# Optimization experiments

Measured on AMD Instinct MI355X. Metric: run time of the kernel, lower is better.

## Reference

```python
import jax, jax.numpy as jnp
import numpy as np

B, S, T, H, VS, VE = 32, 128, 128, 512, 8000, 8000


def _lstm_scan(x_proj, W_hh, bias, h0, c0):
    # x_proj: [L, B, 4H] precomputed input projections; gate order i,f,g,o (PyTorch)
    def step(carry, xp):
        h, c = carry
        gates = xp + h @ W_hh.T + bias  # [B, 4H]
        i, f, g, o = jnp.split(gates, 4, axis=-1)
        c = jax.nn.sigmoid(f) * c + jax.nn.sigmoid(i) * jnp.tanh(g)
        h = jax.nn.sigmoid(o) * jnp.tanh(c)
        return (h, c), h
    (h, c), hs = jax.lax.scan(step, (h0, c0), x_proj)
    return hs, h, c


def setup_inputs() -> dict:
    key = jax.random.key(0)
    ks = jax.random.split(key, 16)
    sc_h = 1.0 / np.sqrt(H)
    u = lambda k, shape: jax.random.uniform(k, shape, jnp.float32, -sc_h, sc_h)
    return {
        "input_batch": jax.random.randint(ks[0], (B, S), 0, VS),
        "output_batch": jax.random.randint(ks[1], (B, T), 0, VE),
        "Wa": u(ks[2], (H, H)), "ba": u(ks[3], (H,)),
        "W1": u(ks[4], (H, 2 * H)), "b1": u(ks[5], (H,)),
        "W2": u(ks[6], (VE, H)), "b2": u(ks[7], (VE,)),
        "We_ih": u(ks[8], (4 * H, VS)), "We_hh": u(ks[9], (4 * H, H)),
        "be_ih": u(ks[10], (4 * H,)), "be_hh": u(ks[11], (4 * H,)),
        "Wd_ih": u(ks[12], (4 * H, VE)), "Wd_hh": u(ks[13], (4 * H, H)),
        "bd_ih": u(ks[14], (4 * H,)), "bd_hh": u(ks[15], (4 * H,)),
    }


def reference(input_batch, output_batch, Wa, ba, W1, b1, W2, b2,
              We_ih, We_hh, be_ih, be_hh, Wd_ih, Wd_hh, bd_ih, bd_hh):
    src = input_batch.T  # [S, B]
    tgt = output_batch.T  # [T, B]
    # one_hot(tok) @ W_ih.T  ==  W_ih.T[tok]  (gather instead of dense one-hot GEMM)
    enc_xp = jnp.take(We_ih.T, src, axis=0)  # [S, B, 4H]
    dec_xp = jnp.take(Wd_ih.T, tgt, axis=0)  # [T, B, 4H]
    h0 = jnp.zeros((B, H), jnp.float32)
    c0 = jnp.zeros((B, H), jnp.float32)
    enc_outputs, h, c = _lstm_scan(enc_xp, We_hh, be_ih + be_hh, h0, c0)  # [S,B,H]
    proj_enc = enc_outputs @ Wa.T + ba  # attn(enc_outputs): [S, B, H]
    dec_bias = bd_ih + bd_hh

    def dec_step(carry, xp):
        h, c = carry
        gates = xp + h @ Wd_hh.T + dec_bias
        i, f, g, o = jnp.split(gates, 4, axis=-1)
        c = jax.nn.sigmoid(f) * c + jax.nn.sigmoid(i) * jnp.tanh(g)
        h = jax.nn.sigmoid(o) * jnp.tanh(c)  # [B, H] == dec_output
        scores = jnp.einsum('sbh,bh->bs', proj_enc, h)  # [B, S]
        w = jax.nn.softmax(scores, axis=1)
        context = jnp.einsum('bs,sbh->bh', w, enc_outputs)  # [B, H]
        hid = jnp.tanh(jnp.concatenate([h, context], axis=1) @ W1.T + b1)
        logits = hid @ W2.T + b2  # [B, VE]
        return (h, c), logits

    _, model = jax.lax.scan(dec_step, (h, c), dec_xp)  # [T, B, VE]
    return jax.nn.softmax(model.transpose(1, 0, 2), axis=2)  # [B, T, VE]
```

## Files before the change

### kernel.cpp

```cpp
#include <hip/hip_runtime.h>
#include <hip/hip_cooperative_groups.h>

#define NB 32
#define NS 128
#define NT 128
#define NH 512
#define NVS 8000
#define NVE 8000

typedef float fx4 __attribute__((ext_vector_type(4)));
typedef short bf16x8 __attribute__((ext_vector_type(8)));
typedef float f32x4 __attribute__((ext_vector_type(4)));

__device__ __forceinline__ float sigm(float x) { return 1.0f / (1.0f + expf(-x)); }

__device__ __forceinline__ fx4 load_cg(const float* p) {
  fx4 v;
  asm volatile("global_load_dwordx4 %0, %1, off sc0 sc1" : "=v"(v) : "v"(p));
  return v;
}
__device__ __forceinline__ void store_cg(float* p, fx4 v) {
  asm volatile("global_store_dwordx4 %0, %1, off sc0 sc1" :: "v"(p), "v"(v) : "memory");
}

__global__ __launch_bounds__(256) void scan_kernel(
    const int* __restrict__ in_tok, const int* __restrict__ out_tok,
    const float* __restrict__ We_ih, const float* __restrict__ We_hh,
    const float* __restrict__ be_ih, const float* __restrict__ be_hh,
    const float* __restrict__ Wd_ih, const float* __restrict__ Wd_hh,
    const float* __restrict__ bd_ih, const float* __restrict__ bd_hh,
    float* __restrict__ h_buf,
    float* __restrict__ enc_out,
    float* __restrict__ dec_h,
    int* __restrict__ flags)
{
  __shared__ float W_lds[16][520];
  __shared__ float h_lds[16 * 516];
  __shared__ float gbuf[16][16];
  __shared__ float c_buf[4][16];
  __shared__ float hstage[16][4];

  const int tid = threadIdx.x;
  const int g   = blockIdx.x;
  const int bg  = g & 1;
  const int mg  = g >> 1;
  const int r   = tid >> 4;
  const int bl  = tid & 15;
  const int b   = bg * 16 + bl;
  const int q   = r >> 2;
  const int i   = r & 3;
  const int j   = q * NH + mg * 4 + i;

  const float bias_e = be_ih[j] + be_hh[j];
  const float bias_d = bd_ih[j] + bd_hh[j];
  const float* Wcol_e = We_ih + (size_t)j * NVS;
  const float* Wcol_d = Wd_ih + (size_t)j * NVE;

  if (tid < 64) c_buf[tid >> 4][tid & 15] = 0.0f;

  {
    const float* Wg = We_hh;
    for (int u = tid; u < 2048; u += 256) {
      const int rr = u >> 7;
      const int k4 = (u & 127) << 2;
      const int jj = (rr >> 2) * NH + mg * 4 + (rr & 3);
      *(float4*)&W_lds[rr][k4] = *(const float4*)(Wg + (size_t)jj * NH + k4);
    }
  }
  __syncthreads();

  for (int s = 0; s < NS + NT; ++s) {
    const bool enc = (s < NS);
    if (s == NS) {
      const float* Wg = Wd_hh;
      for (int u = tid; u < 2048; u += 256) {
        const int rr = u >> 7;
        const int k4 = (u & 127) << 2;
        const int jj = (rr >> 2) * NH + mg * 4 + (rr & 3);
        *(float4*)&W_lds[rr][k4] = *(const float4*)(Wg + (size_t)jj * NH + k4);
      }
      __syncthreads();
    }
    const int st  = enc ? s : s - NS;
    const int tok = enc ? in_tok[b * NS + st] : out_tok[b * NT + st];
    const float xp = enc ? Wcol_e[tok] : Wcol_d[tok];
    const float bias = enc ? bias_e : bias_d;
    const float* Wrow = &W_lds[r][0];

    float acc = 0.0f;
    if (s > 0) {
      if (tid < 128) {
        const int idx = (tid << 1) | bg;
        while (__hip_atomic_load(&flags[idx], __ATOMIC_RELAXED,
                                 __HIP_MEMORY_SCOPE_AGENT) < s)
          __builtin_amdgcn_s_sleep(1);
      }
      __syncthreads();
      const float* hsrc = h_buf + ((s - 1) & 1) * (NB * NH) + bg * 16 * NH;
      fx4 tmp[8];
      #pragma unroll
      for (int it = 0; it < 8; ++it)
        tmp[it] = load_cg(hsrc + ((tid + (it << 8)) << 2));
      asm volatile("s_waitcnt vmcnt(0)" ::: "memory");
      __builtin_amdgcn_sched_barrier(0);
      #pragma unroll
      for (int it = 0; it < 8; ++it) {
        const int u = tid + (it << 8);
        const int bb = u >> 7;
        const int kk = (u & 127) << 2;
        *(fx4*)&h_lds[bb * 516 + kk] = tmp[it];
      }
      __syncthreads();
      const float* hrow = &h_lds[bl * 516];
      #pragma unroll 8
      for (int k = 0; k < NH; k += 4) {
        const float4 hv = *(const float4*)(hrow + k);
        const float4 wv = *(const float4*)(Wrow + k);
        acc += hv.x * wv.x + hv.y * wv.y + hv.z * wv.z + hv.w * wv.w;
      }
    }
    gbuf[r][bl] = acc + xp + bias;
    __syncthreads();

    if (tid < 64) {
      const int ii = tid >> 4;
      const int bb = tid & 15;
      const float gi = gbuf[ii][bb];
      const float gf = gbuf[4 + ii][bb];
      const float gg = gbuf[8 + ii][bb];
      const float go = gbuf[12 + ii][bb];
      const float co = c_buf[ii][bb];
      const float cn = sigm(gf) * co + sigm(gi) * tanhf(gg);
      const float hn = sigm(go) * tanhf(cn);
      c_buf[ii][bb] = cn;
      hstage[bb][ii] = hn;
    }
    __syncthreads();
    if (tid < 16) {
      const fx4 hv = *(const fx4*)&hstage[tid][0];
      const int bglob = bg * 16 + tid;
      store_cg(h_buf + (s & 1) * (NB * NH) + bglob * NH + mg * 4, hv);
      float* dst = enc ? (enc_out + ((size_t)st * NB + bglob) * NH + mg * 4)
                       : (dec_h  + ((size_t)st * NB + bglob) * NH + mg * 4);
      *(fx4*)dst = hv;
    }
    asm volatile("s_waitcnt vmcnt(0)" ::: "memory");
    __syncthreads();
    if (tid == 0)
      __hip_atomic_store(&flags[g], s + 1, __ATOMIC_RELAXED,
                         __HIP_MEMORY_SCOPE_AGENT);
  }
}

template<int TRANSB, int CSWAP, int ACT>
__global__ __launch_bounds__(256) void gemm64(
    const float* __restrict__ A, const float* __restrict__ Bm,
    float* __restrict__ C, const float* __restrict__ bias,
    const float* __restrict__ A2, int ksplit,
    int M, int N, int K, int lda, int ldb, int ldc,
    long batchA, long batchB, long batchC)
{
  __shared__ float As[16][68];
  __shared__ float Bs[16][68];
  const int z = blockIdx.z;
  A += (long)z * batchA;
  if (A2 != nullptr) A2 += (long)z * batchA;
  Bm += (long)z * batchB;
  C  += (long)z * batchC;
  const int m0 = blockIdx.y << 6;
  const int n0 = blockIdx.x << 6;
  const int tid = threadIdx.x;
  const int tx = tid & 15;
  const int ty = tid >> 4;
  float acc[4][4] = {};

  for (int k0 = 0; k0 < K; k0 += 16) {
    {
      const int mrow = tid >> 2;
      const int kcq = (tid & 3) << 2;
      const float* base = A;
      int keff = k0;
      if (A2 != nullptr && k0 >= ksplit) { base = A2; keff = k0 - ksplit; }
      const float4 v = *(const float4*)(base + (long)(m0 + mrow) * lda + keff + kcq);
      As[kcq + 0][mrow] = v.x; As[kcq + 1][mrow] = v.y;
      As[kcq + 2][mrow] = v.z; As[kcq + 3][mrow] = v.w;
    }
    if (TRANSB == 0) {
      const int nrow = tid >> 2;
      const int kcq = (tid & 3) << 2;
      const float4 v = *(const float4*)(Bm + (long)(n0 + nrow) * ldb + k0 + kcq);
      Bs[kcq + 0][nrow] = v.x; Bs[kcq + 1][nrow] = v.y;
      Bs[kcq + 2][nrow] = v.z; Bs[kcq + 3][nrow] = v.w;
    } else {
      const int krow = tid >> 4;
      const int nc = (tid & 15) << 2;
      const float4 v = *(const float4*)(Bm + (long)(k0 + krow) * ldb + n0 + nc);
      *(float4*)&Bs[krow][nc] = v;
    }
    __syncthreads();
    #pragma unroll
    for (int kk = 0; kk < 16; ++kk) {
      const float4 a4 = *(const float4*)&As[kk][ty << 2];
      const float4 b4 = *(const float4*)&Bs[kk][tx << 2];
      const float a[4]  = {a4.x, a4.y, a4.z, a4.w};
      const float bv[4] = {b4.x, b4.y, b4.z, b4.w};
      #pragma unroll
      for (int ii = 0; ii < 4; ++ii)
        #pragma unroll
        for (int jj = 0; jj < 4; ++jj)
          acc[ii][jj] = fmaf(a[ii], bv[jj], acc[ii][jj]);
    }
    __syncthreads();
  }

  const int n = n0 + (tx << 2);
  float4 bb4 = {0.f, 0.f, 0.f, 0.f};
  if (bias) { bb4.x = bias[n]; bb4.y = bias[n + 1]; bb4.z = bias[n + 2]; bb4.w = bias[n + 3]; }
  #pragma unroll
  for (int ii = 0; ii < 4; ++ii) {
    const int mrow = m0 + (ty << 2) + ii;
    float4 o;
    o.x = acc[ii][0] + bb4.x; o.y = acc[ii][1] + bb4.y;
    o.z = acc[ii][2] + bb4.z; o.w = acc[ii][3] + bb4.w;
    if (ACT == 1) { o.x = tanhf(o.x); o.y = tanhf(o.y); o.z = tanhf(o.z); o.w = tanhf(o.w); }
    long orow = mrow;
    if (CSWAP) orow = (long)(mrow & (NB - 1)) * NT + (mrow >> 5);
    *(float4*)(C + orow * (long)ldc + n) = o;
  }
}

template<int CSWAP, int ACT>
__global__ __launch_bounds__(256) void gemm128db(
    const float* __restrict__ A, const float* __restrict__ Bm,
    float* __restrict__ C, const float* __restrict__ bias,
    const float* __restrict__ A2, int ksplit,
    int M, int N, int K, int lda, int ldb, int ldc)
{
  __shared__ float As[2][16][132];
  __shared__ float Bs[2][16][68];
  const int m0 = blockIdx.y << 7;
  const int n0 = blockIdx.x << 6;
  const int tid = threadIdx.x;
  const int tx = tid & 15;
  const int ty = tid >> 4;
  const int mrow = tid >> 1;
  const int kq   = (tid & 1) << 3;
  const int nrow = tid >> 2;
  const int kqb  = (tid & 3) << 2;
  float acc[8][4] = {};

  float4 va0, va1, vb;
  {
    const float* base = A;
    int keff = 0;
    if (A2 != nullptr && 0 >= ksplit) { base = A2; keff = -ksplit; }
    const float* p = base + (long)(m0 + mrow) * lda + keff + kq;
    va0 = *(const float4*)(p);
    va1 = *(const float4*)(p + 4);
    vb  = *(const float4*)(Bm + (long)(n0 + nrow) * ldb + kqb);
  }
  {
    As[0][kq + 0][mrow] = va0.x; As[0][kq + 1][mrow] = va0.y;
    As[0][kq + 2][mrow] = va0.z; As[0][kq + 3][mrow] = va0.w;
    As[0][kq + 4][mrow] = va1.x; As[0][kq + 5][mrow] = va1.y;
    As[0][kq + 6][mrow] = va1.z; As[0][kq + 7][mrow] = va1.w;
    Bs[0][kqb + 0][nrow] = vb.x; Bs[0][kqb + 1][nrow] = vb.y;
    Bs[0][kqb + 2][nrow] = vb.z; Bs[0][kqb + 3][nrow] = vb.w;
  }
  __syncthreads();

  const int T = K >> 4;
  for (int t = 0; t < T; ++t) {
    const int cur = t & 1;
    if (t + 1 < T) {
      const int k0 = (t + 1) << 4;
      const float* base = A;
      int keff = k0;
      if (A2 != nullptr && k0 >= ksplit) { base = A2; keff = k0 - ksplit; }
      const float* p = base + (long)(m0 + mrow) * lda + keff + kq;
      va0 = *(const float4*)(p);
      va1 = *(const float4*)(p + 4);
      vb  = *(const float4*)(Bm + (long)(n0 + nrow) * ldb + k0 + kqb);
    }
    #pragma unroll
    for (int kk = 0; kk < 16; ++kk) {
      const fx4 b4 = *(const fx4*)&Bs[cur][kk][tx << 2];
      const fx4 a0 = *(const fx4*)&As[cur][kk][ty << 3];
      const fx4 a1 = *(const fx4*)&As[cur][kk][(ty << 3) + 4];
      #pragma unroll
      for (int ii = 0; ii < 4; ++ii) {
        #pragma unroll
        for (int jj = 0; jj < 4; ++jj) {
          acc[ii][jj]     = fmaf(a0[ii], b4[jj], acc[ii][jj]);
          acc[ii + 4][jj] = fmaf(a1[ii], b4[jj], acc[ii + 4][jj]);
        }
      }
    }
    if (t + 1 < T) {
      const int nxt = cur ^ 1;
      As[nxt][kq + 0][mrow] = va0.x; As[nxt][kq + 1][mrow] = va0.y;
      As[nxt][kq + 2][mrow] = va0.z; As[nxt][kq + 3][mrow] = va0.w;
      As[nxt][kq + 4][mrow] = va1.x; As[nxt][kq + 5][mrow] = va1.y;
      As[nxt][kq + 6][mrow] = va1.z; As[nxt][kq + 7][mrow] = va1.w;
      Bs[nxt][kqb + 0][nrow] = vb.x; Bs[nxt][kqb + 1][nrow] = vb.y;
      Bs[nxt][kqb + 2][nrow] = vb.z; Bs[nxt][kqb + 3][nrow] = vb.w;
    }
    __syncthreads();
  }

  const int n = n0 + (tx << 2);
  float4 bb4 = {0.f, 0.f, 0.f, 0.f};
  if (bias) { bb4.x = bias[n]; bb4.y = bias[n + 1]; bb4.z = bias[n + 2]; bb4.w = bias[n + 3]; }
  #pragma unroll
  for (int ii = 0; ii < 8; ++ii) {
    const int mr = m0 + (ty << 3) + ii;
    float4 o;
    o.x = acc[ii][0] + bb4.x; o.y = acc[ii][1] + bb4.y;
    o.z = acc[ii][2] + bb4.z; o.w = acc[ii][3] + bb4.w;
    if (ACT == 1) { o.x = tanhf(o.x); o.y = tanhf(o.y); o.z = tanhf(o.z); o.w = tanhf(o.w); }
    long orow = mr;
    if (CSWAP) orow = (long)(mr & (NB - 1)) * NT + (mr >> 5);
    *(float4*)(C + orow * (long)ldc + n) = o;
  }
}

__global__ __launch_bounds__(256) void split_bf16(
    const float* __restrict__ x, unsigned short* __restrict__ hi,
    unsigned short* __restrict__ lo, int n4)
{
  for (int i = blockIdx.x * 256 + threadIdx.x; i < n4; i += gridDim.x * 256) {
    const float4 v = ((const float4*)x)[i];
    float f[4] = {v.x, v.y, v.z, v.w};
    unsigned short hh[4], ll[4];
    #pragma unroll
    for (int jj = 0; jj < 4; ++jj) {
      const unsigned int u = __float_as_uint(f[jj]);
      const unsigned int r = (u + 0x7FFFu + ((u >> 16) & 1u)) >> 16;
      hh[jj] = (unsigned short)r;
      const float hf = __uint_as_float(r << 16);
      const float lf = f[jj] - hf;
      const unsigned int u2 = __float_as_uint(lf);
      const unsigned int r2 = (u2 + 0x7FFFu + ((u2 >> 16) & 1u)) >> 16;
      ll[jj] = (unsigned short)r2;
    }
    ushort4 hv, lv;
    hv.x = hh[0]; hv.y = hh[1]; hv.z = hh[2]; hv.w = hh[3];
    lv.x = ll[0]; lv.y = ll[1]; lv.z = ll[2]; lv.w = ll[3];
    ((ushort4*)hi)[i] = hv;
    ((ushort4*)lo)[i] = lv;
  }
}

__global__ __launch_bounds__(256) void gemm_mfma_logits(
    const unsigned short* __restrict__ Ahi, const unsigned short* __restrict__ Alo,
    const unsigned short* __restrict__ Bhi, const unsigned short* __restrict__ Blo,
    float* __restrict__ C, const float* __restrict__ bias)
{
  const int tid  = threadIdx.x;
  const int wid  = tid >> 6;
  const int lane = tid & 63;
  const int l15  = lane & 15;
  const int kg   = lane >> 4;
  const int m0   = (blockIdx.y << 7) + (wid << 5);
  const int n0   = blockIdx.x << 6;

  const size_t aoff = (size_t)(m0 + l15) * NH + (kg << 3);
  const size_t boff = (size_t)(n0 + l15) * NH + (kg << 3);

  f32x4 acc[2][4];
  #pragma unroll
  for (int fm = 0; fm < 2; ++fm)
    #pragma unroll
    for (int fn = 0; fn < 4; ++fn)
      acc[fm][fn] = (f32x4){0.f, 0.f, 0.f, 0.f};

  for (int k0 = 0; k0 < NH; k0 += 32) {
    bf16x8 ah[2], al[2], bh[4], blv[4];
    #pragma unroll
    for (int fm = 0; fm < 2; ++fm) {
      ah[fm] = *(const bf16x8*)(Ahi + aoff + (size_t)(fm << 4) * NH + k0);
      al[fm] = *(const bf16x8*)(Alo + aoff + (size_t)(fm << 4) * NH + k0);
    }
    #pragma unroll
    for (int fn = 0; fn < 4; ++fn) {
      bh[fn]  = *(const bf16x8*)(Bhi + boff + (size_t)(fn << 4) * NH + k0);
      blv[fn] = *(const bf16x8*)(Blo + boff + (size_t)(fn << 4) * NH + k0);
    }
    #pragma unroll
    for (int fm = 0; fm < 2; ++fm) {
      #pragma unroll
      for (int fn = 0; fn < 4; ++fn) {
        acc[fm][fn] = __builtin_amdgcn_mfma_f32_16x16x32_bf16(
            ah[fm], bh[fn], acc[fm][fn], 0, 0, 0);
        acc[fm][fn] = __builtin_amdgcn_mfma_f32_16x16x32_bf16(
            ah[fm], blv[fn], acc[fm][fn], 0, 0, 0);
        acc[fm][fn] = __builtin_amdgcn_mfma_f32_16x16x32_bf16(
            al[fm], bh[fn], acc[fm][fn], 0, 0, 0);
      }
    }
  }

  #pragma unroll
  for (int fm = 0; fm < 2; ++fm) {
    #pragma unroll
    for (int fn = 0; fn < 4; ++fn) {
      const int n = n0 + (fn << 4) + l15;
      const float bb = bias[n];
      #pragma unroll
      for (int rg = 0; rg < 4; ++rg) {
        const int m = m0 + (fm << 4) + (kg << 2) + rg;
        const long orow = (long)(m & (NB - 1)) * NT + (m >> 5);
        C[orow * NVE + n] = acc[fm][fn][rg] + bb;
      }
    }
  }
}

__global__ __launch_bounds__(128) void softmax_s(float* __restrict__ sc) {
  const long row = blockIdx.x;
  float* p = sc + row * NS;
  const float x = p[threadIdx.x];
  float mx = x;
  for (int o = 32; o; o >>= 1) mx = fmaxf(mx, __shfl_xor(mx, o));
  __shared__ float r0[2], r1[2];
  const int w = threadIdx.x >> 6;
  if ((threadIdx.x & 63) == 0) r0[w] = mx;
  __syncthreads();
  mx = fmaxf(r0[0], r0[1]);
  const float e = expf(x - mx);
  float sum = e;
  for (int o = 32; o; o >>= 1) sum += __shfl_xor(sum, o);
  if ((threadIdx.x & 63) == 0) r1[w] = sum;
  __syncthreads();
  sum = r1[0] + r1[1];
  p[threadIdx.x] = e / sum;
}

__global__ __launch_bounds__(256) void softmax_v(float* __restrict__ out) {
  const long row = blockIdx.x;
  float* p = out + row * NVE;
  float v[32];
  float mx = -1e30f;
  #pragma unroll
  for (int it = 0; it < 32; ++it) {
    const int idx = (it << 8) + threadIdx.x;
    v[it] = (idx < NVE) ? p[idx] : -1e30f;
    mx = fmaxf(mx, v[it]);
  }
  for (int o = 32; o; o >>= 1) mx = fmaxf(mx, __shfl_xor(mx, o));
  __shared__ float red[4], red2[4];
  const int w = threadIdx.x >> 6;
  if ((threadIdx.x & 63) == 0) red[w] = mx;
  __syncthreads();
  mx = fmaxf(fmaxf(red[0], red[1]), fmaxf(red[2], red[3]));
  float sum = 0.0f;
  #pragma unroll
  for (int it = 0; it < 32; ++it) {
    const int idx = (it << 8) + threadIdx.x;
    if (idx < NVE) { v[it] = expf(v[it] - mx); sum += v[it]; }
  }
  for (int o = 32; o; o >>= 1) sum += __shfl_xor(sum, o);
  if ((threadIdx.x & 63) == 0) red2[w] = sum;
  __syncthreads();
  sum = red2[0] + red2[1] + red2[2] + red2[3];
  const float inv = 1.0f / sum;
  #pragma unroll
  for (int it = 0; it < 32; ++it) {
    const int idx = (it << 8) + threadIdx.x;
    if (idx < NVE) p[idx] = v[it] * inv;
  }
}

extern "C" void kernel_launch(void* const* d_in, const int* in_sizes, int n_in,
                              void* d_out, int out_size, void* d_ws, size_t ws_size,
                              hipStream_t stream) {
  const int*   in_tok = (const int*)d_in[0];
  const int*   out_tok = (const int*)d_in[1];
  const float* Wa    = (const float*)d_in[2];
  const float* ba    = (const float*)d_in[3];
  const float* W1    = (const float*)d_in[4];
  const float* b1    = (const float*)d_in[5];
  const float* W2    = (const float*)d_in[6];
  const float* b2    = (const float*)d_in[7];
  const float* We_ih = (const float*)d_in[8];
  const float* We_hh = (const float*)d_in[9];
  const float* be_ih = (const float*)d_in[10];
  const float* be_hh = (const float*)d_in[11];
  const float* Wd_ih = (const float*)d_in[12];
  const float* Wd_hh = (const float*)d_in[13];
  const float* bd_ih = (const float*)d_in[14];
  const float* bd_hh = (const float*)d_in[15];

  float* ws      = (float*)d_ws;
  float* h_buf   = ws;
  float* enc_out = ws + 32768;
  float* dec_h   = ws + 2129920;
  float* proj    = ws + 4227072;
  float* scores  = ws + 6324224;
  float* ctx     = ws + 6848512;
  float* hid     = ws + 8945664;
  int*   flags   = (int*)(ws + 11042816);
  float* out     = (float*)d_out;

  unsigned short* hid_hi = (unsigned short*)proj;
  unsigned short* hid_lo = (unsigned short*)(proj + 1048576);
  unsigned short* W2_hi  = (unsigned short*)enc_out;
  unsigned short* W2_lo  = (unsigned short*)(enc_out + 2048000);

  (void)hipMemsetAsync((void*)flags, 0, 256 * sizeof(int), stream);

  {
    void* args[14];
    args[0] = (void*)&in_tok; args[1] = (void*)&out_tok;
    args[2] = (void*)&We_ih;  args[3] = (void*)&We_hh;
    args[4] = (void*)&be_ih;  args[5] = (void*)&be_hh;
    args[6] = (void*)&Wd_ih;  args[7] = (void*)&Wd_hh;
    args[8] = (void*)&bd_ih;  args[9] = (void*)&bd_hh;
    args[10] = (void*)&h_buf; args[11] = (void*)&enc_out; args[12] = (void*)&dec_h;
    args[13] = (void*)&flags;
    (void)hipLaunchCooperativeKernel((void*)scan_kernel, dim3(256), dim3(256), args, 0, stream);
  }

  gemm128db<0,0><<<dim3(8,32,1), 256, 0, stream>>>(
      enc_out, Wa, proj, ba, nullptr, 1 << 30,
      4096, 512, 512, 512, 512, 512);

  gemm64<0,0,0><<<dim3(2,2,NB), 256, 0, stream>>>(
      dec_h, proj, scores, nullptr, nullptr, 1 << 30,
      NT, NS, NH, NB * NH, NB * NH, NB * NS,
      (long)NH, (long)NH, (long)NS);

  softmax_s<<<dim3(NT * NB), 128, 0, stream>>>(scores);

  gemm64<1,0,0><<<dim3(8,2,NB), 256, 0, stream>>>(
      scores, enc_out, ctx, nullptr, nullptr, 1 << 30,
      NT, NH, NS, NB * NS, NB * NH, NB * NH,
      (long)NS, (long)NH, (long)NH);

  gemm128db<0,1><<<dim3(8,32,1), 256, 0, stream>>>(
      dec_h, W1, hid, b1, ctx, 512,
      4096, 512, 1024, 512, 1024, 512);

  split_bf16<<<dim3(2048), 256, 0, stream>>>(hid, hid_hi, hid_lo, 4096 * 512 / 4);
  split_bf16<<<dim3(2048), 256, 0, stream>>>(W2, W2_hi, W2_lo, NVE * 512 / 4);

  gemm_mfma_logits<<<dim3(125, 32), 256, 0, stream>>>(
      hid_hi, hid_lo, W2_hi, W2_lo, out, b2);

  softmax_v<<<dim3(NB * NT), 256, 0, stream>>>(out);
}
```

Before: 2.156 ms.

## Fuse bf16 hi/lo split into hidden GEMM epilogue and stage W2 tiles in LDS

```diff
diff --git a/kernel.cpp b/kernel.cpp
--- a/kernel.cpp
+++ b/kernel.cpp
@@ -13,6 +13,11 @@
 typedef float f32x4 __attribute__((ext_vector_type(4)));
 
 __device__ __forceinline__ float sigm(float x) { return 1.0f / (1.0f + expf(-x)); }
+
+__device__ __forceinline__ unsigned short bf16_rne(float x) {
+  const unsigned int u = __float_as_uint(x);
+  return (unsigned short)((u + 0x7FFFu + ((u >> 16) & 1u)) >> 16);
+}
 
 __device__ __forceinline__ fx4 load_cg(const float* p) {
   fx4 v;
@@ -229,12 +234,13 @@
   }
 }
 
-template<int CSWAP, int ACT>
+template<int CSWAP, int ACT, int OUT>
 __global__ __launch_bounds__(256) void gemm128db(
     const float* __restrict__ A, const float* __restrict__ Bm,
     float* __restrict__ C, const float* __restrict__ bias,
     const float* __restrict__ A2, int ksplit,
-    int M, int N, int K, int lda, int ldb, int ldc)
+    int M, int N, int K, int lda, int ldb, int ldc,
+    unsigned short* __restrict__ outHi, unsigned short* __restrict__ outLo)
 {
   __shared__ float As[2][16][132];
   __shared__ float Bs[2][16][68];
@@ -320,7 +326,26 @@
     if (ACT == 1) { o.x = tanhf(o.x); o.y = tanhf(o.y); o.z = tanhf(o.z); o.w = tanhf(o.w); }
     long orow = mr;
     if (CSWAP) orow = (long)(mr & (NB - 1)) * NT + (mr >> 5);
-    *(float4*)(C + orow * (long)ldc + n) = o;
+    if (OUT == 2) {
+      float f[4] = {o.x, o.y, o.z, o.w};
+      ushort4 hh, ll;
+      unsigned short* hp = (unsigned short*)&hh;
+      unsigned short* lp = (unsigned short*)&ll;
+      #pragma unroll
+      for (int jj = 0; jj < 4; ++jj) {
+        const unsigned int u = __float_as_uint(f[jj]);
+        const unsigned int rv = (u + 0x7FFFu + ((u >> 16) & 1u)) >> 16;
+        hp[jj] = (unsigned short)rv;
+        const float hf = __uint_as_float(rv << 16);
+        const float lf = f[jj] - hf;
+        const unsigned int u2 = __float_as_uint(lf);
+        lp[jj] = (unsigned short)((u2 + 0x7FFFu + ((u2 >> 16) & 1u)) >> 16);
+      }
+      *(ushort4*)(outHi + orow * (long)ldc + n) = hh;
+      *(ushort4*)(outLo + orow * (long)ldc + n) = ll;
+    } else {
+      *(float4*)(C + orow * (long)ldc + n) = o;
+    }
   }
 }
 
@@ -356,6 +381,8 @@
     const unsigned short* __restrict__ Bhi, const unsigned short* __restrict__ Blo,
     float* __restrict__ C, const float* __restrict__ bias)
 {
+  __shared__ unsigned short BsH[64 * 32];
+  __shared__ unsigned short BsL[64 * 32];
   const int tid  = threadIdx.x;
   const int wid  = tid >> 6;
   const int lane = tid & 63;
@@ -365,7 +392,8 @@
   const int n0   = blockIdx.x << 6;
 
   const size_t aoff = (size_t)(m0 + l15) * NH + (kg << 3);
-  const size_t boff = (size_t)(n0 + l15) * NH + (kg << 3);
+  const int srow = tid >> 2;
+  const int scol = (tid & 3) << 3;
 
   f32x4 acc[2][4];
   #pragma unroll
@@ -375,27 +403,31 @@
       acc[fm][fn] = (f32x4){0.f, 0.f, 0.f, 0.f};
 
   for (int k0 = 0; k0 < NH; k0 += 32) {
-    bf16x8 ah[2], al[2], bh[4], blv[4];
+    __syncthreads();
+    *(bf16x8*)&BsH[srow * 32 + scol] =
+        *(const bf16x8*)(Bhi + (size_t)(n0 + srow) * NH + k0 + scol);
+    *(bf16x8*)&BsL[srow * 32 + scol] =
+        *(const bf16x8*)(Blo + (size_t)(n0 + srow) * NH + k0 + scol);
+    __syncthreads();
+
+    bf16x8 ah[2], al[2];
     #pragma unroll
     for (int fm = 0; fm < 2; ++fm) {
       ah[fm] = *(const bf16x8*)(Ahi + aoff + (size_t)(fm << 4) * NH + k0);
       al[fm] = *(const bf16x8*)(Alo + aoff + (size_t)(fm << 4) * NH + k0);
     }
     #pragma unroll
-    for (int fn = 0; fn < 4; ++fn) {
-      bh[fn]  = *(const bf16x8*)(Bhi + boff + (size_t)(fn << 4) * NH + k0);
-      blv[fn] = *(const bf16x8*)(Blo + boff + (size_t)(fn << 4) * NH + k0);
-    }
-    #pragma unroll
     for (int fm = 0; fm < 2; ++fm) {
       #pragma unroll
       for (int fn = 0; fn < 4; ++fn) {
+        const bf16x8 bh  = *(const bf16x8*)&BsH[(((fn << 4) + l15) << 5) + (kg << 3)];
+        const bf16x8 blv = *(const bf16x8*)&BsL[(((fn << 4) + l15) << 5) + (kg << 3)];
         acc[fm][fn] = __builtin_amdgcn_mfma_f32_16x16x32_bf16(
-            ah[fm], bh[fn], acc[fm][fn], 0, 0, 0);
+            ah[fm], bh, acc[fm][fn], 0, 0, 0);
         acc[fm][fn] = __builtin_amdgcn_mfma_f32_16x16x32_bf16(
-            ah[fm], blv[fn], acc[fm][fn], 0, 0, 0);
+            ah[fm], blv, acc[fm][fn], 0, 0, 0);
         acc[fm][fn] = __builtin_amdgcn_mfma_f32_16x16x32_bf16(
-            al[fm], bh[fn], acc[fm][fn], 0, 0, 0);
+            al[fm], bh, acc[fm][fn], 0, 0, 0);
       }
     }
   }
@@ -521,9 +553,9 @@
     (void)hipLaunchCooperativeKernel((void*)scan_kernel, dim3(256), dim3(256), args, 0, stream);
   }
 
-  gemm128db<0,0><<<dim3(8,32,1), 256, 0, stream>>>(
+  gemm128db<0,0,0><<<dim3(8,32,1), 256, 0, stream>>>(
       enc_out, Wa, proj, ba, nullptr, 1 << 30,
-      4096, 512, 512, 512, 512, 512);
+      4096, 512, 512, 512, 512, 512, nullptr, nullptr);
 
   gemm64<0,0,0><<<dim3(2,2,NB), 256, 0, stream>>>(
       dec_h, proj, scores, nullptr, nullptr, 1 << 30,
@@ -537,11 +569,10 @@
       NT, NH, NS, NB * NS, NB * NH, NB * NH,
       (long)NS, (long)NH, (long)NH);
 
-  gemm128db<0,1><<<dim3(8,32,1), 256, 0, stream>>>(
-      dec_h, W1, hid, b1, ctx, 512,
-      4096, 512, 1024, 512, 1024, 512);
-
-  split_bf16<<<dim3(2048), 256, 0, stream>>>(hid, hid_hi, hid_lo, 4096 * 512 / 4);
+  gemm128db<0,1,2><<<dim3(8,32,1), 256, 0, stream>>>(
+      dec_h, W1, nullptr, b1, ctx, 512,
+      4096, 512, 1024, 512, 1024, 512, hid_hi, hid_lo);
+
   split_bf16<<<dim3(2048), 256, 0, stream>>>(W2, W2_hi, W2_lo, NVE * 512 / 4);
 
   gemm_mfma_logits<<<dim3(125, 32), 256, 0, stream>>>(
```

Result: faster. 1.984 ms (-8.0%).
